# Performance work log

Measured on AMD Instinct MI355X. Metric: run time of the kernel, lower is better.

## Reference

```python
import jax, jax.numpy as jnp
import numpy as np

B, K, DIM = 8192, 256, 1024


def setup_inputs() -> dict:
    key = jax.random.key(0)
    k1, k2, k3 = jax.random.split(key, 3)
    x = jax.random.normal(k1, (B, DIM), dtype=jnp.float32)
    centers = jax.random.uniform(k2, (K, DIM), dtype=jnp.float32)
    # torch init: D = 0.2 * rand + 0.9
    D = 0.2 * jax.random.uniform(k3, (K, DIM), dtype=jnp.float32) + 0.9
    return {"x": x, "centers": centers, "D": D}


def reference(x, centers, D):
    # Per-class axis-aligned (diagonal) covariance
    D_abs = jnp.abs(D) + 1e-4                      # [K, DIM]
    D_inv = 1.0 / D_abs                            # [K, DIM]
    log_det = jnp.sum(jnp.log(D_abs), axis=1)      # [K]
    det_scale_factor = -0.5 * log_det
    det_scale_safe = jnp.exp(det_scale_factor - jnp.max(det_scale_factor))  # [K]

    # dist_sq[b,k] = sum_d (x[b,d]-c[k,d])^2 * D_inv[k,d]
    # Expanded quadratic form avoids materializing the [B,K,DIM] diff tensor.
    x2 = jnp.einsum('bd,kd->bk', x * x, D_inv)             # [B, K]
    xc = jnp.einsum('bd,kd->bk', x, centers * D_inv)       # [B, K]
    c2 = jnp.sum(centers * centers * D_inv, axis=1)        # [K]
    dist_sq = x2 - 2.0 * xc + c2[None, :]                  # [B, K]

    # Gaussian path (isCauchy=False)
    expo = -0.5 * dist_sq
    expo_safe = expo - jnp.max(expo, axis=-1, keepdims=True)
    numer_safe = det_scale_safe[None, :] * jnp.exp(expo_safe)
    denom_safe = jnp.sum(numer_safe, axis=1, keepdims=True)
    resp = numer_safe / denom_safe                         # [B, K]
    return resp
```

## Files before the change

kernel.cpp:

```cpp
#include <hip/hip_runtime.h>

typedef _Float16 f16x8 __attribute__((ext_vector_type(8)));
typedef _Float16 f16x4 __attribute__((ext_vector_type(4)));
typedef float f32x4 __attribute__((ext_vector_type(4)));

#define B_N 8192
#define K_N 256
#define DIM_N 1024

__global__ __launch_bounds__(256) void prep_w(const float* __restrict__ Dm,
                                              const float* __restrict__ Cm,
                                              _Float16* __restrict__ Uf,
                                              _Float16* __restrict__ Wf,
                                              float* __restrict__ c2,
                                              float* __restrict__ dsf) {
    const int k = blockIdx.x, t = threadIdx.x;
    const int d = t * 4;
    const float4 dv = *(const float4*)(Dm + (size_t)k * DIM_N + d);
    const float4 cv = *(const float4*)(Cm + (size_t)k * DIM_N + d);
    float dd[4] = {dv.x, dv.y, dv.z, dv.w};
    float cc[4] = {cv.x, cv.y, cv.z, cv.w};
    f16x4 uo, wo;
    float llog = 0.f, lc2 = 0.f;
#pragma unroll
    for (int i = 0; i < 4; ++i) {
        float da = fabsf(dd[i]) + 1e-4f;
        float dinv = 1.0f / da;
        llog += logf(da);
        lc2 += cc[i] * cc[i] * dinv;
        uo[i] = (_Float16)(dinv - 1.0f);
        wo[i] = (_Float16)(-2.0f * cc[i] * dinv);
    }
    *(f16x4*)(Uf + (size_t)k * DIM_N + d) = uo;
    *(f16x4*)(Wf + (size_t)k * DIM_N + d) = wo;
#pragma unroll
    for (int m = 1; m <= 32; m <<= 1) {
        llog += __shfl_xor(llog, m, 64);
        lc2 += __shfl_xor(lc2, m, 64);
    }
    __shared__ float sl[4], sc[4];
    if ((t & 63) == 0) { sl[t >> 6] = llog; sc[t >> 6] = lc2; }
    __syncthreads();
    if (t == 0) {
        dsf[k] = -0.5f * (sl[0] + sl[1] + sl[2] + sl[3]);
        c2[k] = sc[0] + sc[1] + sc[2] + sc[3];
    }
}

__global__ __launch_bounds__(256) void prep2(const float* __restrict__ dsf,
                                             float* __restrict__ dss) {
    const int t = threadIdx.x;
    const float v = dsf[t];
    float m = v;
#pragma unroll
    for (int msk = 1; msk <= 32; msk <<= 1) m = fmaxf(m, __shfl_xor(m, msk, 64));
    __shared__ float sm[4];
    if ((t & 63) == 0) sm[t >> 6] = m;
    __syncthreads();
    m = fmaxf(fmaxf(sm[0], sm[1]), fmaxf(sm[2], sm[3]));
    dss[t] = expf(v - m);
}

__global__ __launch_bounds__(512, 1)
void gmm_gemm(const float* __restrict__ x,
              const _Float16* __restrict__ Uf,
              const _Float16* __restrict__ Wf,
              float* __restrict__ P0, float* __restrict__ P1) {
    __shared__ __align__(16) char lds[65536];

    const int tid = threadIdx.x;
    const int wave = tid >> 6, lane = tid & 63, l15 = lane & 15, g = lane >> 4;
    const int wr = wave >> 2, wc = wave & 3;

    const int bid = blockIdx.x;
    const int xcd = bid & 7, i2 = bid >> 3;
    const int rowp = (i2 >> 2) * 8 + xcd;
    const int tc = i2 & 3;
    const int type = tc & 1, colp = tc >> 1;
    const int bRow = rowp * 128;
    const int bCol = colp * 128;

    const _Float16* __restrict__ Wsrc = type ? Wf : Uf;
    const bool sq = (type == 0);

    const int r_ = tid >> 2, q_ = tid & 3;
    const float* xp = x + (size_t)(bRow + r_) * DIM_N + q_ * 16;
    const _Float16* wp = Wsrc + (size_t)(bCol + r_) * DIM_N + q_ * 16;

    int cwr[2];
#pragma unroll
    for (int j = 0; j < 2; ++j) {
        const int s = q_ * 2 + j;
        cwr[j] = s * 2048 + ((r_ ^ s) & 127) * 16;
    }
    int aRd[4][2], bRd[2][2];
#pragma unroll
    for (int k2 = 0; k2 < 2; ++k2) {
        const int s = k2 * 4 + g;
#pragma unroll
        for (int m = 0; m < 4; ++m) {
            const int row = wr * 64 + m * 16 + l15;
            aRd[m][k2] = s * 2048 + ((row ^ s) & 127) * 16;
        }
#pragma unroll
        for (int n = 0; n < 2; ++n) {
            const int col = wc * 32 + n * 16 + l15;
            bRd[n][k2] = s * 2048 + ((col ^ s) & 127) * 16;
        }
    }

    f32x4 acc[4][2];
#pragma unroll
    for (int m = 0; m < 4; ++m)
#pragma unroll
        for (int n = 0; n < 2; ++n) {
            f32x4 z = {0.f, 0.f, 0.f, 0.f};
            acc[m][n] = z;
        }

    float4 xv[2][4];
    f16x8 wv[2][2];

    auto loadX = [&](int bank, int c) {
#pragma unroll
        for (int q = 0; q < 4; ++q) xv[bank][q] = *(const float4*)(xp + c * 64 + q * 4);
    };
    auto loadB = [&](int bank, int c) {
        wv[bank][0] = *(const f16x8*)(wp + c * 64);
        wv[bank][1] = *(const f16x8*)(wp + c * 64 + 8);
    };
    auto stage = [&](int abase, int bbase, int bank) {
        _Float16 h[16];
#pragma unroll
        for (int q = 0; q < 4; ++q) {
            float f4[4] = {xv[bank][q].x, xv[bank][q].y, xv[bank][q].z, xv[bank][q].w};
#pragma unroll
            for (int i = 0; i < 4; ++i) {
                const float f = f4[i];
                const float t2 = sq ? f : 1.0f;
                h[q * 4 + i] = (_Float16)(f * t2);
            }
        }
        *(f16x8*)(lds + abase + cwr[0]) = *(const f16x8*)&h[0];
        *(f16x8*)(lds + abase + cwr[1]) = *(const f16x8*)&h[8];
        *(f16x8*)(lds + bbase + cwr[0]) = wv[bank][0];
        *(f16x8*)(lds + bbase + cwr[1]) = wv[bank][1];
    };

    loadX(0, 0); loadB(0, 0);
    loadX(1, 1); loadB(1, 1);
    stage(0, 32768, 0);
    asm volatile("s_waitcnt lgkmcnt(0)" ::: "memory");
    __builtin_amdgcn_s_barrier();
    __builtin_amdgcn_sched_barrier(0);

#pragma unroll
    for (int c = 0; c < 16; ++c) {
        const int cur = c & 1, nxt = cur ^ 1;
        const int aCur = cur * 16384, aNxt = nxt * 16384;
        const int bCur = 32768 + cur * 16384, bNxt = 32768 + nxt * 16384;
        if (c < 14) { loadX(cur, c + 2); loadB(cur, c + 2); }
        f16x8 af[4][2], bf[2][2];
#pragma unroll
        for (int k2 = 0; k2 < 2; ++k2) {
#pragma unroll
            for (int m = 0; m < 4; ++m) af[m][k2] = *(const f16x8*)(lds + aCur + aRd[m][k2]);
#pragma unroll
            for (int n = 0; n < 2; ++n) bf[n][k2] = *(const f16x8*)(lds + bCur + bRd[n][k2]);
        }
        __builtin_amdgcn_s_setprio(1);
#pragma unroll
        for (int m = 0; m < 4; ++m)
#pragma unroll
            for (int n = 0; n < 2; ++n)
#pragma unroll
                for (int k2 = 0; k2 < 2; ++k2)
                    acc[m][n] = __builtin_amdgcn_mfma_f32_16x16x32_f16(af[m][k2], bf[n][k2], acc[m][n], 0, 0, 0);
        __builtin_amdgcn_s_setprio(0);
        if (c < 15) {
            stage(aNxt, bNxt, nxt);
            asm volatile("s_waitcnt lgkmcnt(0)" ::: "memory");
            __builtin_amdgcn_s_barrier();
            __builtin_amdgcn_sched_barrier(0);
        }
    }

    float* __restrict__ P = type ? P1 : P0;
#pragma unroll
    for (int m = 0; m < 4; ++m) {
        const int rb = bRow + wr * 64 + m * 16 + g * 4;
        const int cb = bCol + wc * 32 + l15;
#pragma unroll
        for (int j = 0; j < 4; ++j) {
            float* p = P + (size_t)(rb + j) * K_N + cb;
            p[0] = acc[m][0][j];
            p[16] = acc[m][1][j];
        }
    }
}

__global__ __launch_bounds__(256)
void gmm_soft(float* __restrict__ S, const float* __restrict__ P1,
              const float* __restrict__ c2g, const float* __restrict__ dssg) {
    const int tid = threadIdx.x;
    const int wave = tid >> 6, lane = tid & 63;
    const int r = blockIdx.x * 4 + wave;
    const int k0 = lane * 4;
    float4 s0 = *(const float4*)(S + (size_t)r * K_N + k0);
    float4 s1 = *(const float4*)(P1 + (size_t)r * K_N + k0);
    float4 cv = *(const float4*)(c2g + k0);
    float4 dv = *(const float4*)(dssg + k0);
    float e[4] = {-0.5f * (s0.x + s1.x + cv.x), -0.5f * (s0.y + s1.y + cv.y),
                  -0.5f * (s0.z + s1.z + cv.z), -0.5f * (s0.w + s1.w + cv.w)};
    float dvv[4] = {dv.x, dv.y, dv.z, dv.w};
    float m = fmaxf(fmaxf(e[0], e[1]), fmaxf(e[2], e[3]));
#pragma unroll
    for (int msk = 1; msk <= 32; msk <<= 1) m = fmaxf(m, __shfl_xor(m, msk, 64));
    float p[4], sum = 0.f;
#pragma unroll
    for (int j = 0; j < 4; ++j) {
        p[j] = dvv[j] * __expf(e[j] - m);
        sum += p[j];
    }
#pragma unroll
    for (int msk = 1; msk <= 32; msk <<= 1) sum += __shfl_xor(sum, msk, 64);
    const float inv = 1.0f / sum;
    *(float4*)(S + (size_t)r * K_N + k0) = make_float4(p[0] * inv, p[1] * inv, p[2] * inv, p[3] * inv);
}

extern "C" void kernel_launch(void* const* d_in, const int* in_sizes, int n_in,
                              void* d_out, int out_size, void* d_ws, size_t ws_size,
                              hipStream_t stream) {
    const float* x = (const float*)d_in[0];
    const float* cen = (const float*)d_in[1];
    const float* Dm = (const float*)d_in[2];
    float* out = (float*)d_out;

    char* ws = (char*)d_ws;
    _Float16* Uf = (_Float16*)(ws);
    _Float16* Wf = (_Float16*)(ws + 524288);
    float* P1 = (float*)(ws + 1048576);
    float* c2 = (float*)(ws + 9437184);
    float* dsf = (float*)(ws + 9438208);
    float* dss = (float*)(ws + 9439232);

    prep_w<<<dim3(K_N), dim3(256), 0, stream>>>(Dm, cen, Uf, Wf, c2, dsf);
    prep2<<<dim3(1), dim3(256), 0, stream>>>(dsf, dss);
    gmm_gemm<<<dim3(256), dim3(512), 0, stream>>>(x, Uf, Wf, out, P1);
    gmm_soft<<<dim3(B_N / 4), dim3(256), 0, stream>>>(out, P1, c2, dss);
}
```

Measured before the change: 33.22 us.

## Fuse both quadratic-form GEMMs into one accumulator and fold per-class constants

```diff
diff --git a/kernel.cpp b/kernel.cpp
--- a/kernel.cpp
+++ b/kernel.cpp
@@ -12,8 +12,7 @@
                                               const float* __restrict__ Cm,
                                               _Float16* __restrict__ Uf,
                                               _Float16* __restrict__ Wf,
-                                              float* __restrict__ c2,
-                                              float* __restrict__ dsf) {
+                                              float* __restrict__ ec) {
     const int k = blockIdx.x, t = threadIdx.x;
     const int d = t * 4;
     const float4 dv = *(const float4*)(Dm + (size_t)k * DIM_N + d);
@@ -33,123 +32,104 @@
     }
     *(f16x4*)(Uf + (size_t)k * DIM_N + d) = uo;
     *(f16x4*)(Wf + (size_t)k * DIM_N + d) = wo;
-#pragma unroll
-    for (int m = 1; m <= 32; m <<= 1) {
-        llog += __shfl_xor(llog, m, 64);
-        lc2 += __shfl_xor(lc2, m, 64);
-    }
-    __shared__ float sl[4], sc[4];
-    if ((t & 63) == 0) { sl[t >> 6] = llog; sc[t >> 6] = lc2; }
+    float both = llog + lc2;
+#pragma unroll
+    for (int m = 1; m <= 32; m <<= 1) both += __shfl_xor(both, m, 64);
+    __shared__ float sb[4];
+    if ((t & 63) == 0) sb[t >> 6] = both;
     __syncthreads();
-    if (t == 0) {
-        dsf[k] = -0.5f * (sl[0] + sl[1] + sl[2] + sl[3]);
-        c2[k] = sc[0] + sc[1] + sc[2] + sc[3];
-    }
-}
-
-__global__ __launch_bounds__(256) void prep2(const float* __restrict__ dsf,
-                                             float* __restrict__ dss) {
-    const int t = threadIdx.x;
-    const float v = dsf[t];
-    float m = v;
-#pragma unroll
-    for (int msk = 1; msk <= 32; msk <<= 1) m = fmaxf(m, __shfl_xor(m, msk, 64));
-    __shared__ float sm[4];
-    if ((t & 63) == 0) sm[t >> 6] = m;
-    __syncthreads();
-    m = fmaxf(fmaxf(sm[0], sm[1]), fmaxf(sm[2], sm[3]));
-    dss[t] = expf(v - m);
+    if (t == 0) ec[k] = -0.5f * (sb[0] + sb[1] + sb[2] + sb[3]);
 }
 
 __global__ __launch_bounds__(512, 1)
 void gmm_gemm(const float* __restrict__ x,
               const _Float16* __restrict__ Uf,
               const _Float16* __restrict__ Wf,
-              float* __restrict__ P0, float* __restrict__ P1) {
-    __shared__ __align__(16) char lds[65536];
+              float* __restrict__ S) {
+    __shared__ __align__(16) char lds[98304];
 
     const int tid = threadIdx.x;
     const int wave = tid >> 6, lane = tid & 63, l15 = lane & 15, g = lane >> 4;
     const int wr = wave >> 2, wc = wave & 3;
 
     const int bid = blockIdx.x;
-    const int xcd = bid & 7, i2 = bid >> 3;
-    const int rowp = (i2 >> 2) * 8 + xcd;
-    const int tc = i2 & 3;
-    const int type = tc & 1, colp = tc >> 1;
-    const int bRow = rowp * 128;
+    const int xcd = bid & 7, idx = bid >> 3;
+    const int colp = idx & 1;
+    const int rowp = (idx >> 1) * 8 + xcd;
+    const int bRow = rowp * 64;
     const int bCol = colp * 128;
 
-    const _Float16* __restrict__ Wsrc = type ? Wf : Uf;
-    const bool sq = (type == 0);
-
-    const int r_ = tid >> 2, q_ = tid & 3;
-    const float* xp = x + (size_t)(bRow + r_) * DIM_N + q_ * 16;
-    const _Float16* wp = Wsrc + (size_t)(bCol + r_) * DIM_N + q_ * 16;
-
-    int cwr[2];
+    const int xrow = tid >> 3, xs = tid & 7;
+    const float* xp = x + (size_t)(bRow + xrow) * DIM_N + xs * 8;
+    const int aWr = xs * 1024 + (((xrow ^ xs) & 63) << 4);
+    const int wrow = tid >> 2, wq = tid & 3;
+    const _Float16* up = Uf + (size_t)(bCol + wrow) * DIM_N + wq * 16;
+    const _Float16* wp = Wf + (size_t)(bCol + wrow) * DIM_N + wq * 16;
+    int bWr[2];
 #pragma unroll
     for (int j = 0; j < 2; ++j) {
-        const int s = q_ * 2 + j;
-        cwr[j] = s * 2048 + ((r_ ^ s) & 127) * 16;
-    }
-    int aRd[4][2], bRd[2][2];
+        const int s = wq * 2 + j;
+        bWr[j] = s * 2048 + (((wrow ^ s) & 127) << 4);
+    }
+
+    int aRd[2][2], bRd[2][2];
 #pragma unroll
     for (int k2 = 0; k2 < 2; ++k2) {
         const int s = k2 * 4 + g;
 #pragma unroll
-        for (int m = 0; m < 4; ++m) {
-            const int row = wr * 64 + m * 16 + l15;
-            aRd[m][k2] = s * 2048 + ((row ^ s) & 127) * 16;
+        for (int m = 0; m < 2; ++m) {
+            const int row = wr * 32 + m * 16 + l15;
+            aRd[m][k2] = s * 1024 + (((row ^ s) & 63) << 4);
         }
 #pragma unroll
         for (int n = 0; n < 2; ++n) {
             const int col = wc * 32 + n * 16 + l15;
-            bRd[n][k2] = s * 2048 + ((col ^ s) & 127) * 16;
-        }
-    }
-
-    f32x4 acc[4][2];
-#pragma unroll
-    for (int m = 0; m < 4; ++m)
+            bRd[n][k2] = s * 2048 + (((col ^ s) & 127) << 4);
+        }
+    }
+
+    f32x4 acc[2][2];
+#pragma unroll
+    for (int m = 0; m < 2; ++m)
 #pragma unroll
         for (int n = 0; n < 2; ++n) {
             f32x4 z = {0.f, 0.f, 0.f, 0.f};
             acc[m][n] = z;
         }
 
-    float4 xv[2][4];
-    f16x8 wv[2][2];
+    float4 xv[2][2];
+    f16x8 uv[2][2], wv[2][2];
 
     auto loadX = [&](int bank, int c) {
-#pragma unroll
-        for (int q = 0; q < 4; ++q) xv[bank][q] = *(const float4*)(xp + c * 64 + q * 4);
+        xv[bank][0] = *(const float4*)(xp + c * 64);
+        xv[bank][1] = *(const float4*)(xp + c * 64 + 4);
     };
-    auto loadB = [&](int bank, int c) {
+    auto loadW = [&](int bank, int c) {
+        uv[bank][0] = *(const f16x8*)(up + c * 64);
+        uv[bank][1] = *(const f16x8*)(up + c * 64 + 8);
         wv[bank][0] = *(const f16x8*)(wp + c * 64);
         wv[bank][1] = *(const f16x8*)(wp + c * 64 + 8);
     };
-    auto stage = [&](int abase, int bbase, int bank) {
-        _Float16 h[16];
-#pragma unroll
-        for (int q = 0; q < 4; ++q) {
-            float f4[4] = {xv[bank][q].x, xv[bank][q].y, xv[bank][q].z, xv[bank][q].w};
-#pragma unroll
-            for (int i = 0; i < 4; ++i) {
-                const float f = f4[i];
-                const float t2 = sq ? f : 1.0f;
-                h[q * 4 + i] = (_Float16)(f * t2);
-            }
-        }
-        *(f16x8*)(lds + abase + cwr[0]) = *(const f16x8*)&h[0];
-        *(f16x8*)(lds + abase + cwr[1]) = *(const f16x8*)&h[8];
-        *(f16x8*)(lds + bbase + cwr[0]) = wv[bank][0];
-        *(f16x8*)(lds + bbase + cwr[1]) = wv[bank][1];
+    auto stage = [&](int base, int bank) {
+        float f[8] = {xv[bank][0].x, xv[bank][0].y, xv[bank][0].z, xv[bank][0].w,
+                      xv[bank][1].x, xv[bank][1].y, xv[bank][1].z, xv[bank][1].w};
+        _Float16 h2[8], hx[8];
+#pragma unroll
+        for (int i = 0; i < 8; ++i) {
+            h2[i] = (_Float16)(f[i] * f[i]);
+            hx[i] = (_Float16)f[i];
+        }
+        *(f16x8*)(lds + base + aWr) = *(const f16x8*)&h2[0];
+        *(f16x8*)(lds + base + 8192 + aWr) = *(const f16x8*)&hx[0];
+        *(f16x8*)(lds + base + 16384 + bWr[0]) = uv[bank][0];
+        *(f16x8*)(lds + base + 16384 + bWr[1]) = uv[bank][1];
+        *(f16x8*)(lds + base + 32768 + bWr[0]) = wv[bank][0];
+        *(f16x8*)(lds + base + 32768 + bWr[1]) = wv[bank][1];
     };
 
-    loadX(0, 0); loadB(0, 0);
-    loadX(1, 1); loadB(1, 1);
-    stage(0, 32768, 0);
+    loadX(0, 0); loadW(0, 0);
+    loadX(1, 1); loadW(1, 1);
+    stage(0, 0);
     asm volatile("s_waitcnt lgkmcnt(0)" ::: "memory");
     __builtin_amdgcn_s_barrier();
     __builtin_amdgcn_sched_barrier(0);
@@ -157,42 +137,48 @@
 #pragma unroll
     for (int c = 0; c < 16; ++c) {
         const int cur = c & 1, nxt = cur ^ 1;
-        const int aCur = cur * 16384, aNxt = nxt * 16384;
-        const int bCur = 32768 + cur * 16384, bNxt = 32768 + nxt * 16384;
-        if (c < 14) { loadX(cur, c + 2); loadB(cur, c + 2); }
-        f16x8 af[4][2], bf[2][2];
+        const int bCur = cur * 49152, bNxt = nxt * 49152;
+        if (c < 14) { loadX(cur, c + 2); loadW(cur, c + 2); }
+        f16x8 a2f[2][2], axf[2][2], buf[2][2], bwf[2][2];
 #pragma unroll
         for (int k2 = 0; k2 < 2; ++k2) {
 #pragma unroll
-            for (int m = 0; m < 4; ++m) af[m][k2] = *(const f16x8*)(lds + aCur + aRd[m][k2]);
-#pragma unroll
-            for (int n = 0; n < 2; ++n) bf[n][k2] = *(const f16x8*)(lds + bCur + bRd[n][k2]);
+            for (int m = 0; m < 2; ++m) {
+                a2f[m][k2] = *(const f16x8*)(lds + bCur + aRd[m][k2]);
+                axf[m][k2] = *(const f16x8*)(lds + bCur + 8192 + aRd[m][k2]);
+            }
+#pragma unroll
+            for (int n = 0; n < 2; ++n) {
+                buf[n][k2] = *(const f16x8*)(lds + bCur + 16384 + bRd[n][k2]);
+                bwf[n][k2] = *(const f16x8*)(lds + bCur + 32768 + bRd[n][k2]);
+            }
         }
         __builtin_amdgcn_s_setprio(1);
 #pragma unroll
-        for (int m = 0; m < 4; ++m)
+        for (int m = 0; m < 2; ++m)
 #pragma unroll
             for (int n = 0; n < 2; ++n)
 #pragma unroll
-                for (int k2 = 0; k2 < 2; ++k2)
-                    acc[m][n] = __builtin_amdgcn_mfma_f32_16x16x32_f16(af[m][k2], bf[n][k2], acc[m][n], 0, 0, 0);
+                for (int k2 = 0; k2 < 2; ++k2) {
+                    acc[m][n] = __builtin_amdgcn_mfma_f32_16x16x32_f16(a2f[m][k2], buf[n][k2], acc[m][n], 0, 0, 0);
+                    acc[m][n] = __builtin_amdgcn_mfma_f32_16x16x32_f16(axf[m][k2], bwf[n][k2], acc[m][n], 0, 0, 0);
+                }
         __builtin_amdgcn_s_setprio(0);
         if (c < 15) {
-            stage(aNxt, bNxt, nxt);
+            stage(bNxt, nxt);
             asm volatile("s_waitcnt lgkmcnt(0)" ::: "memory");
             __builtin_amdgcn_s_barrier();
             __builtin_amdgcn_sched_barrier(0);
         }
     }
 
-    float* __restrict__ P = type ? P1 : P0;
-#pragma unroll
-    for (int m = 0; m < 4; ++m) {
-        const int rb = bRow + wr * 64 + m * 16 + g * 4;
+#pragma unroll
+    for (int m = 0; m < 2; ++m) {
+        const int rb = bRow + wr * 32 + m * 16 + g * 4;
         const int cb = bCol + wc * 32 + l15;
 #pragma unroll
         for (int j = 0; j < 4; ++j) {
-            float* p = P + (size_t)(rb + j) * K_N + cb;
+            float* p = S + (size_t)(rb + j) * K_N + cb;
             p[0] = acc[m][0][j];
             p[16] = acc[m][1][j];
         }
@@ -200,26 +186,22 @@
 }
 
 __global__ __launch_bounds__(256)
-void gmm_soft(float* __restrict__ S, const float* __restrict__ P1,
-              const float* __restrict__ c2g, const float* __restrict__ dssg) {
+void gmm_soft(float* __restrict__ S, const float* __restrict__ ecg) {
     const int tid = threadIdx.x;
     const int wave = tid >> 6, lane = tid & 63;
     const int r = blockIdx.x * 4 + wave;
     const int k0 = lane * 4;
-    float4 s0 = *(const float4*)(S + (size_t)r * K_N + k0);
-    float4 s1 = *(const float4*)(P1 + (size_t)r * K_N + k0);
-    float4 cv = *(const float4*)(c2g + k0);
-    float4 dv = *(const float4*)(dssg + k0);
-    float e[4] = {-0.5f * (s0.x + s1.x + cv.x), -0.5f * (s0.y + s1.y + cv.y),
-                  -0.5f * (s0.z + s1.z + cv.z), -0.5f * (s0.w + s1.w + cv.w)};
-    float dvv[4] = {dv.x, dv.y, dv.z, dv.w};
+    float4 s = *(const float4*)(S + (size_t)r * K_N + k0);
+    float4 cv = *(const float4*)(ecg + k0);
+    float e[4] = {fmaf(-0.5f, s.x, cv.x), fmaf(-0.5f, s.y, cv.y),
+                  fmaf(-0.5f, s.z, cv.z), fmaf(-0.5f, s.w, cv.w)};
     float m = fmaxf(fmaxf(e[0], e[1]), fmaxf(e[2], e[3]));
 #pragma unroll
     for (int msk = 1; msk <= 32; msk <<= 1) m = fmaxf(m, __shfl_xor(m, msk, 64));
     float p[4], sum = 0.f;
 #pragma unroll
     for (int j = 0; j < 4; ++j) {
-        p[j] = dvv[j] * __expf(e[j] - m);
+        p[j] = __expf(e[j] - m);
         sum += p[j];
     }
 #pragma unroll
@@ -239,13 +221,9 @@
     char* ws = (char*)d_ws;
     _Float16* Uf = (_Float16*)(ws);
     _Float16* Wf = (_Float16*)(ws + 524288);
-    float* P1 = (float*)(ws + 1048576);
-    float* c2 = (float*)(ws + 9437184);
-    float* dsf = (float*)(ws + 9438208);
-    float* dss = (float*)(ws + 9439232);
-
-    prep_w<<<dim3(K_N), dim3(256), 0, stream>>>(Dm, cen, Uf, Wf, c2, dsf);
-    prep2<<<dim3(1), dim3(256), 0, stream>>>(dsf, dss);
-    gmm_gemm<<<dim3(256), dim3(512), 0, stream>>>(x, Uf, Wf, out, P1);
-    gmm_soft<<<dim3(B_N / 4), dim3(256), 0, stream>>>(out, P1, c2, dss);
-}
+    float* ec = (float*)(ws + 1048576);
+
+    prep_w<<<dim3(K_N), dim3(256), 0, stream>>>(Dm, cen, Uf, Wf, ec);
+    gmm_gemm<<<dim3(256), dim3(512), 0, stream>>>(x, Uf, Wf, out);
+    gmm_soft<<<dim3(B_N / 4), dim3(256), 0, stream>>>(out, ec);
+}
```

Result: slower. 36.05 us (+8.5%).
